# Performance work log

Measured on AMD Instinct MI355X. Metric: run time of the kernel, lower is better.

Reference implementation:

```python
import jax, jax.numpy as jnp
import numpy as np

SEQ, BS, H, I, E = 2048, 4, 2048, 4096, 8


def setup_inputs() -> dict:
    key = jax.random.key(0)
    ks = jax.random.split(key, 5)
    s = 0.02
    return {
        "hidden_states": jax.random.normal(ks[0], (SEQ, BS, H), dtype=jnp.float32),
        "router_w": jax.random.normal(ks[1], (H, E), dtype=jnp.float32) * s,
        "gate_w": jax.random.normal(ks[2], (E, H, I), dtype=jnp.float32) * s,
        "up_w": jax.random.normal(ks[3], (E, H, I), dtype=jnp.float32) * s,
        "down_w": jax.random.normal(ks[4], (E, I, H), dtype=jnp.float32) * s,
    }


def reference(hidden_states, router_w, gate_w, up_w, down_w):
    # Router: [S,B,H] @ [H,E] -> [S,B,E]; top-1 routing (num_experts_per_tok == 1)
    router_logits = jnp.einsum("sbh,he->sbe", hidden_states, router_w)
    routing_indices = jnp.argmax(router_logits, axis=-1)  # [S,B]
    # sigmoid routing weights are computed but NOT applied in the original combine
    routing_weights = jax.nn.sigmoid(jnp.max(router_logits, axis=-1))  # noqa: F841

    out = jnp.zeros_like(hidden_states)
    for e in range(E):  # small fixed expert count
        mask = (routing_indices == e)[..., None]  # [S,B,1]
        g = jnp.einsum("sbh,hi->sbi", hidden_states, gate_w[e])
        u = jnp.einsum("sbh,hi->sbi", hidden_states, up_w[e])
        y = jnp.einsum("sbi,ih->sbh", jax.nn.silu(g) * u, down_w[e])
        out = out + jnp.where(mask, y, jnp.zeros((), out.dtype))
    return out
```

## Files before the change

### kernel.cpp

```cpp
#include <hip/hip_runtime.h>
#include <hip/hip_bf16.h>

#define T_TOKENS 8192
#define H_DIM 2048
#define I_DIM 4096
#define E_EXP 8
#define PAD_ROWS 9216

typedef __bf16 bf16x8 __attribute__((ext_vector_type(8)));
typedef float floatx4 __attribute__((ext_vector_type(4)));
typedef unsigned short ushort8 __attribute__((ext_vector_type(8)));

__device__ __forceinline__ unsigned short f2bf(float f) {
  union { float f; unsigned int i; } c; c.f = f;
  unsigned int x = c.i;
  unsigned int r = x + 0x7fffu + ((x >> 16) & 1u);
  return (unsigned short)(r >> 16);
}

__device__ __forceinline__ float bf2float(unsigned short u) {
  union { unsigned int i; float f; } c; c.i = ((unsigned int)u) << 16;
  return c.f;
}

__device__ __forceinline__ void gload_lds16(const void* g, void* l) {
  __builtin_amdgcn_global_load_lds(
      (const __attribute__((address_space(1))) void*)g,
      (__attribute__((address_space(3))) void*)l, 16, 0, 0);
}

__global__ __launch_bounds__(256) void xcvt_kernel(const float* __restrict__ x,
                                                   unsigned short* __restrict__ xb,
                                                   int* __restrict__ hdr) {
  if (blockIdx.x == 0 && threadIdx.x < 32) hdr[threadIdx.x] = 0;
  int i = (blockIdx.x * 256 + threadIdx.x) * 4;
  floatx4 v = *(const floatx4*)(x + i);
  unsigned short o0 = f2bf(v[0]), o1 = f2bf(v[1]), o2 = f2bf(v[2]), o3 = f2bf(v[3]);
  ushort4 o; o.x = o0; o.y = o1; o.z = o2; o.w = o3;
  *(ushort4*)(xb + i) = o;
}

__global__ __launch_bounds__(256) void router_kernel(const float* __restrict__ x,
                                                     const float* __restrict__ rw,
                                                     int* __restrict__ idx,
                                                     int* __restrict__ hdr) {
  int lane = threadIdx.x & 63;
  int t = blockIdx.x * 4 + (threadIdx.x >> 6);
  const float* xr = x + (size_t)t * H_DIM;
  float acc[8];
#pragma unroll
  for (int e = 0; e < 8; ++e) acc[e] = 0.f;
  for (int i = lane; i < H_DIM; i += 64) {
    float h = xr[i];
    floatx4 r0 = *(const floatx4*)(rw + i * 8);
    floatx4 r1 = *(const floatx4*)(rw + i * 8 + 4);
#pragma unroll
    for (int e = 0; e < 4; ++e) { acc[e] += h * r0[e]; acc[e + 4] += h * r1[e]; }
  }
#pragma unroll
  for (int off = 32; off > 0; off >>= 1)
#pragma unroll
    for (int e = 0; e < 8; ++e) acc[e] += __shfl_xor(acc[e], off, 64);
  if (lane == 0) {
    int best = 0; float bv = acc[0];
#pragma unroll
    for (int e = 1; e < 8; ++e) if (acc[e] > bv) { bv = acc[e]; best = e; }
    idx[t] = best;
    atomicAdd(&hdr[best], 1);
  }
}

__global__ __launch_bounds__(256) void setup_kernel(int* __restrict__ hdr,
                                                    int* __restrict__ rows) {
  if (threadIdx.x == 0) {
    int b = 0;
    for (int e = 0; e < 8; ++e) {
      hdr[16 + e] = b;
      b += ((hdr[e] + 127) >> 7) << 7;
    }
  }
  for (int i = threadIdx.x; i < PAD_ROWS; i += 256) rows[i] = -1;
}

__global__ __launch_bounds__(256) void scatter_kernel(const int* __restrict__ idx,
                                                      int* __restrict__ hdr,
                                                      int* __restrict__ rows) {
  int t = blockIdx.x * 256 + threadIdx.x;
  int e = idx[t];
  int p = atomicAdd(&hdr[8 + e], 1);
  rows[hdr[16 + e] + p] = t;
}

template <int K, int N>
__global__ __launch_bounds__(256) void wtrans_kernel(const float* __restrict__ W,
                                                     unsigned short* __restrict__ Wt) {
  const int e = blockIdx.z;
  const int bn = blockIdx.x * 256;
  const int bk = blockIdx.y * 64;
  const float* Wp = W + (size_t)e * K * N;
  unsigned short* Wtp = Wt + (size_t)e * N * K;
  const int tid = threadIdx.x;
  const int n0 = (tid & 31) * 8;
  const int k0 = (tid >> 5) * 8;

  const float* src = Wp + (size_t)(bk + k0) * N + bn + n0;
  floatx4 a[8][2];
#pragma unroll
  for (int kk = 0; kk < 8; ++kk) {
    a[kk][0] = *(const floatx4*)(src + (size_t)kk * N);
    a[kk][1] = *(const floatx4*)(src + (size_t)kk * N + 4);
  }
  unsigned short* dst = Wtp + (size_t)(bn + n0) * K + bk + k0;
#pragma unroll
  for (int nn = 0; nn < 8; ++nn) {
    ushort8 o;
#pragma unroll
    for (int kk = 0; kk < 8; ++kk) o[kk] = f2bf(a[kk][nn >> 2][nn & 3]);
    *(ushort8*)(dst + (size_t)nn * K) = o;
  }
}

__global__ __launch_bounds__(256, 2) void moe_gemm_gu(
    const unsigned short* __restrict__ A,
    const unsigned short* __restrict__ Bg,
    const unsigned short* __restrict__ Bu,
    const int* __restrict__ hdr,
    const int* __restrict__ rows,
    unsigned short* __restrict__ inter) {
  const int e = blockIdx.z;
  const int cnt = hdr[e];
  if ((int)blockIdx.y * 128 >= cnt) return;
  const int seg = hdr[16 + e];

  const int tid = threadIdx.x;
  const int lane = tid & 63;
  const int wv = tid >> 6;
  const int wm = (wv & 1) * 64;
  const int wn = (wv >> 1) * 64;
  const int q = lane >> 4;
  const int l15 = lane & 15;

  __shared__ unsigned short sA[128 * 64];
  __shared__ unsigned short sBg[128 * 64];
  __shared__ unsigned short sBu[128 * 64];

  const int lr = lane >> 3;
  const int colsw = (lane & 7) ^ lr;
  const unsigned short* aptr[4];
  const unsigned short* bgptr[4];
  const unsigned short* buptr[4];
  const unsigned short* BgE = Bg + (size_t)e * I_DIM * H_DIM;
  const unsigned short* BuE = Bu + (size_t)e * I_DIM * H_DIM;
#pragma unroll
  for (int j = 0; j < 4; ++j) {
    const int R = j * 32 + wv * 8 + lr;
    int ar = rows[seg + blockIdx.y * 128 + R];
    if (ar < 0) ar = 0;
    aptr[j] = A + (size_t)ar * H_DIM + colsw * 8;
    bgptr[j] = BgE + (size_t)(blockIdx.x * 128 + R) * H_DIM + colsw * 8;
    buptr[j] = BuE + (size_t)(blockIdx.x * 128 + R) * H_DIM + colsw * 8;
  }

  floatx4 accg[4][4], accu[4][4];
#pragma unroll
  for (int a = 0; a < 4; ++a)
#pragma unroll
    for (int b = 0; b < 4; ++b) {
      accg[a][b] = (floatx4){0.f, 0.f, 0.f, 0.f};
      accu[a][b] = (floatx4){0.f, 0.f, 0.f, 0.f};
    }

  for (int kt = 0; kt < H_DIM; kt += 64) {
#pragma unroll
    for (int j = 0; j < 4; ++j) {
      gload_lds16(aptr[j] + kt, sA + (j * 32 + wv * 8) * 64);
      gload_lds16(bgptr[j] + kt, sBg + (j * 32 + wv * 8) * 64);
      gload_lds16(buptr[j] + kt, sBu + (j * 32 + wv * 8) * 64);
    }
    __syncthreads();
#pragma unroll
    for (int ks = 0; ks < 64; ks += 32) {
      const int sbase = ks >> 3;
      bf16x8 af[4], bfr[4];
#pragma unroll
      for (int fm = 0; fm < 4; ++fm) {
        const int ra = wm + fm * 16 + l15;
        af[fm] = __builtin_bit_cast(bf16x8,
            *(const ushort8*)(sA + ra * 64 + (((q + sbase) ^ (ra & 7)) << 3)));
      }
#pragma unroll
      for (int fn = 0; fn < 4; ++fn) {
        const int rb = wn + fn * 16 + l15;
        bfr[fn] = __builtin_bit_cast(bf16x8,
            *(const ushort8*)(sBg + rb * 64 + (((q + sbase) ^ (rb & 7)) << 3)));
      }
#pragma unroll
      for (int fm = 0; fm < 4; ++fm)
#pragma unroll
        for (int fn = 0; fn < 4; ++fn)
          accg[fm][fn] = __builtin_amdgcn_mfma_f32_16x16x32_bf16(af[fm], bfr[fn],
                                                                 accg[fm][fn], 0, 0, 0);
#pragma unroll
      for (int fn = 0; fn < 4; ++fn) {
        const int rb = wn + fn * 16 + l15;
        bfr[fn] = __builtin_bit_cast(bf16x8,
            *(const ushort8*)(sBu + rb * 64 + (((q + sbase) ^ (rb & 7)) << 3)));
      }
#pragma unroll
      for (int fm = 0; fm < 4; ++fm)
#pragma unroll
        for (int fn = 0; fn < 4; ++fn)
          accu[fm][fn] = __builtin_amdgcn_mfma_f32_16x16x32_bf16(af[fm], bfr[fn],
                                                                 accu[fm][fn], 0, 0, 0);
    }
    __syncthreads();
  }

#pragma unroll
  for (int fm = 0; fm < 4; ++fm)
#pragma unroll
    for (int fn = 0; fn < 4; ++fn)
#pragma unroll
      for (int rr = 0; rr < 4; ++rr) {
        const int row = wm + fm * 16 + q * 4 + rr;
        const int col = wn + fn * 16 + l15;
        const int gm = blockIdx.y * 128 + row;
        const int gn = blockIdx.x * 128 + col;
        const float g = accg[fm][fn][rr];
        const float u = accu[fm][fn][rr];
        const float s = g / (1.f + __expf(-g));
        inter[(size_t)(seg + gm) * I_DIM + gn] = f2bf(s * u);
      }
}

__global__ __launch_bounds__(256) void moe_gemm_down(
    const unsigned short* __restrict__ A,
    const unsigned short* __restrict__ Bt,
    const int* __restrict__ hdr,
    const int* __restrict__ rows,
    float* __restrict__ outp) {
  const int e = blockIdx.z;
  const int cnt = hdr[e];
  if ((int)blockIdx.y * 128 >= cnt) return;
  const int seg = hdr[16 + e];

  const int tid = threadIdx.x;
  const int lane = tid & 63;
  const int wv = tid >> 6;
  const int wm = (wv & 1) * 64;
  const int wn = (wv >> 1) * 64;
  const int q = lane >> 4;
  const int l15 = lane & 15;

  __shared__ unsigned short sA[128 * 64];
  __shared__ unsigned short sB[128 * 64];

  const int lr = lane >> 3;
  const int colsw = (lane & 7) ^ lr;
  const unsigned short* aptr[4];
  const unsigned short* bptr[4];
  const unsigned short* Be = Bt + (size_t)e * H_DIM * I_DIM;
#pragma unroll
  for (int j = 0; j < 4; ++j) {
    const int R = j * 32 + wv * 8 + lr;
    aptr[j] = A + (size_t)(seg + blockIdx.y * 128 + R) * I_DIM + colsw * 8;
    bptr[j] = Be + (size_t)(blockIdx.x * 128 + R) * I_DIM + colsw * 8;
  }

  floatx4 acc[4][4];
#pragma unroll
  for (int a = 0; a < 4; ++a)
#pragma unroll
    for (int b = 0; b < 4; ++b) acc[a][b] = (floatx4){0.f, 0.f, 0.f, 0.f};

  for (int kt = 0; kt < I_DIM; kt += 64) {
#pragma unroll
    for (int j = 0; j < 4; ++j) {
      gload_lds16(aptr[j] + kt, sA + (j * 32 + wv * 8) * 64);
      gload_lds16(bptr[j] + kt, sB + (j * 32 + wv * 8) * 64);
    }
    __syncthreads();
#pragma unroll
    for (int ks = 0; ks < 64; ks += 32) {
      const int sbase = ks >> 3;
      bf16x8 af[4], bfr[4];
#pragma unroll
      for (int fm = 0; fm < 4; ++fm) {
        const int ra = wm + fm * 16 + l15;
        af[fm] = __builtin_bit_cast(bf16x8,
            *(const ushort8*)(sA + ra * 64 + (((q + sbase) ^ (ra & 7)) << 3)));
      }
#pragma unroll
      for (int fn = 0; fn < 4; ++fn) {
        const int rb = wn + fn * 16 + l15;
        bfr[fn] = __builtin_bit_cast(bf16x8,
            *(const ushort8*)(sB + rb * 64 + (((q + sbase) ^ (rb & 7)) << 3)));
      }
#pragma unroll
      for (int fm = 0; fm < 4; ++fm)
#pragma unroll
        for (int fn = 0; fn < 4; ++fn)
          acc[fm][fn] = __builtin_amdgcn_mfma_f32_16x16x32_bf16(af[fm], bfr[fn],
                                                                acc[fm][fn], 0, 0, 0);
    }
    __syncthreads();
  }

#pragma unroll
  for (int fm = 0; fm < 4; ++fm)
#pragma unroll
    for (int fn = 0; fn < 4; ++fn)
#pragma unroll
      for (int rr = 0; rr < 4; ++rr) {
        const int row = wm + fm * 16 + q * 4 + rr;
        const int col = wn + fn * 16 + l15;
        const int gm = blockIdx.y * 128 + row;
        const int gn = blockIdx.x * 128 + col;
        const int tok = rows[seg + gm];
        if (tok >= 0) outp[(size_t)tok * H_DIM + gn] = acc[fm][fn][rr];
      }
}

extern "C" void kernel_launch(void* const* d_in, const int* in_sizes, int n_in,
                              void* d_out, int out_size, void* d_ws, size_t ws_size,
                              hipStream_t stream) {
  const float* hidden   = (const float*)d_in[0];
  const float* router_w = (const float*)d_in[1];
  const float* gate_w   = (const float*)d_in[2];
  const float* up_w     = (const float*)d_in[3];
  const float* down_w   = (const float*)d_in[4];
  float* out = (float*)d_out;

  char* ws = (char*)d_ws;
  int* hdr  = (int*)ws;
  int* idx  = (int*)(ws + 1024);
  int* rows = (int*)(ws + 33792);
  unsigned short* x_bf  = (unsigned short*)(ws + 70656);
  unsigned short* inter = (unsigned short*)(ws + 33625088);
  unsigned short* W1    = (unsigned short*)(ws + 109122560);
  unsigned short* W2    = (unsigned short*)(ws + 243340288);
  unsigned short* downt = W1;

  xcvt_kernel<<<T_TOKENS * H_DIM / 1024, 256, 0, stream>>>(hidden, x_bf, hdr);
  router_kernel<<<T_TOKENS / 4, 256, 0, stream>>>(hidden, router_w, idx, hdr);
  setup_kernel<<<1, 256, 0, stream>>>(hdr, rows);
  scatter_kernel<<<T_TOKENS / 256, 256, 0, stream>>>(idx, hdr, rows);

  wtrans_kernel<H_DIM, I_DIM><<<dim3(I_DIM / 256, H_DIM / 64, E_EXP), 256, 0, stream>>>(gate_w, W1);
  wtrans_kernel<H_DIM, I_DIM><<<dim3(I_DIM / 256, H_DIM / 64, E_EXP), 256, 0, stream>>>(up_w, W2);

  moe_gemm_gu<<<dim3(I_DIM / 128, 64, E_EXP), 256, 0, stream>>>(
      x_bf, W1, W2, hdr, rows, inter);

  wtrans_kernel<I_DIM, H_DIM><<<dim3(H_DIM / 256, I_DIM / 64, E_EXP), 256, 0, stream>>>(down_w, downt);
  moe_gemm_down<<<dim3(H_DIM / 128, 64, E_EXP), 256, 0, stream>>>(
      inter, downt, hdr, rows, out);
}
```

Before: 1.549 ms.

## Transpose weights via LDS tile and widen down-GEMM tile to 128x256

The weight transpose/convert kernel now stages a 64x64 tile in swizzled shared memory, so global reads are coalesced float4 rows and global writes are coalesced 16-byte rows. The old version wrote scattered 16-byte chunks with a large stride. The down-projection GEMM now computes two 128-column B tiles per block, reusing each A tile across twice the output width. This halves A reloads and block count. It raises register and LDS use (two accumulator sets, extra sB buffer) and sets launch bounds to 2 waves per EU, which may limit occupancy.

```diff
diff --git a/kernel.cpp b/kernel.cpp
--- a/kernel.cpp
+++ b/kernel.cpp
@@ -94,29 +94,42 @@
 template <int K, int N>
 __global__ __launch_bounds__(256) void wtrans_kernel(const float* __restrict__ W,
                                                      unsigned short* __restrict__ Wt) {
+  __shared__ unsigned short tile[64 * 64];
   const int e = blockIdx.z;
-  const int bn = blockIdx.x * 256;
+  const int bn = blockIdx.x * 64;
   const int bk = blockIdx.y * 64;
-  const float* Wp = W + (size_t)e * K * N;
-  unsigned short* Wtp = Wt + (size_t)e * N * K;
+  const float* Wp = W + (size_t)e * K * N + (size_t)bk * N + bn;
+  unsigned short* Wtp = Wt + (size_t)e * N * K + (size_t)bn * K + bk;
   const int tid = threadIdx.x;
-  const int n0 = (tid & 31) * 8;
-  const int k0 = (tid >> 5) * 8;
-
-  const float* src = Wp + (size_t)(bk + k0) * N + bn + n0;
-  floatx4 a[8][2];
-#pragma unroll
-  for (int kk = 0; kk < 8; ++kk) {
-    a[kk][0] = *(const floatx4*)(src + (size_t)kk * N);
-    a[kk][1] = *(const floatx4*)(src + (size_t)kk * N + 4);
-  }
-  unsigned short* dst = Wtp + (size_t)(bn + n0) * K + bk + k0;
-#pragma unroll
-  for (int nn = 0; nn < 8; ++nn) {
-    ushort8 o;
-#pragma unroll
-    for (int kk = 0; kk < 8; ++kk) o[kk] = f2bf(a[kk][nn >> 2][nn & 3]);
-    *(ushort8*)(dst + (size_t)nn * K) = o;
+
+  {
+    const int kq = tid >> 4;
+    const int nq = tid & 15;
+    floatx4 v[4];
+#pragma unroll
+    for (int i = 0; i < 4; ++i)
+      v[i] = *(const floatx4*)(Wp + (size_t)(kq * 4 + i) * N + nq * 4);
+    const int s16 = kq >> 1;
+    const int half = kq & 1;
+#pragma unroll
+    for (int j = 0; j < 4; ++j) {
+      const int n = nq * 4 + j;
+      ushort4 t;
+      t.x = f2bf(v[0][j]); t.y = f2bf(v[1][j]);
+      t.z = f2bf(v[2][j]); t.w = f2bf(v[3][j]);
+      *(ushort4*)(tile + n * 64 + ((s16 ^ (n & 7)) << 3) + half * 4) = t;
+    }
+  }
+  __syncthreads();
+  {
+    const int kc = tid & 7;
+    const int nr = tid >> 3;
+#pragma unroll
+    for (int it = 0; it < 2; ++it) {
+      const int n = it * 32 + nr;
+      ushort8 o = *(const ushort8*)(tile + n * 64 + ((kc ^ (n & 7)) << 3));
+      *(ushort8*)(Wtp + (size_t)n * K + kc * 8) = o;
+    }
   }
 }
 
@@ -233,7 +246,7 @@
       }
 }
 
-__global__ __launch_bounds__(256) void moe_gemm_down(
+__global__ __launch_bounds__(256, 2) void moe_gemm_down(
     const unsigned short* __restrict__ A,
     const unsigned short* __restrict__ Bt,
     const int* __restrict__ hdr,
@@ -253,31 +266,38 @@
   const int l15 = lane & 15;
 
   __shared__ unsigned short sA[128 * 64];
-  __shared__ unsigned short sB[128 * 64];
+  __shared__ unsigned short sB0[128 * 64];
+  __shared__ unsigned short sB1[128 * 64];
 
   const int lr = lane >> 3;
   const int colsw = (lane & 7) ^ lr;
   const unsigned short* aptr[4];
-  const unsigned short* bptr[4];
+  const unsigned short* b0ptr[4];
+  const unsigned short* b1ptr[4];
   const unsigned short* Be = Bt + (size_t)e * H_DIM * I_DIM;
 #pragma unroll
   for (int j = 0; j < 4; ++j) {
     const int R = j * 32 + wv * 8 + lr;
-    aptr[j] = A + (size_t)(seg + blockIdx.y * 128 + R) * I_DIM + colsw * 8;
-    bptr[j] = Be + (size_t)(blockIdx.x * 128 + R) * I_DIM + colsw * 8;
-  }
-
-  floatx4 acc[4][4];
+    aptr[j]  = A + (size_t)(seg + blockIdx.y * 128 + R) * I_DIM + colsw * 8;
+    b0ptr[j] = Be + (size_t)(blockIdx.x * 256 + R) * I_DIM + colsw * 8;
+    b1ptr[j] = Be + (size_t)(blockIdx.x * 256 + 128 + R) * I_DIM + colsw * 8;
+  }
+
+  floatx4 acc0[4][4], acc1[4][4];
 #pragma unroll
   for (int a = 0; a < 4; ++a)
 #pragma unroll
-    for (int b = 0; b < 4; ++b) acc[a][b] = (floatx4){0.f, 0.f, 0.f, 0.f};
+    for (int b = 0; b < 4; ++b) {
+      acc0[a][b] = (floatx4){0.f, 0.f, 0.f, 0.f};
+      acc1[a][b] = (floatx4){0.f, 0.f, 0.f, 0.f};
+    }
 
   for (int kt = 0; kt < I_DIM; kt += 64) {
 #pragma unroll
     for (int j = 0; j < 4; ++j) {
       gload_lds16(aptr[j] + kt, sA + (j * 32 + wv * 8) * 64);
-      gload_lds16(bptr[j] + kt, sB + (j * 32 + wv * 8) * 64);
+      gload_lds16(b0ptr[j] + kt, sB0 + (j * 32 + wv * 8) * 64);
+      gload_lds16(b1ptr[j] + kt, sB1 + (j * 32 + wv * 8) * 64);
     }
     __syncthreads();
 #pragma unroll
@@ -294,14 +314,26 @@
       for (int fn = 0; fn < 4; ++fn) {
         const int rb = wn + fn * 16 + l15;
         bfr[fn] = __builtin_bit_cast(bf16x8,
-            *(const ushort8*)(sB + rb * 64 + (((q + sbase) ^ (rb & 7)) << 3)));
+            *(const ushort8*)(sB0 + rb * 64 + (((q + sbase) ^ (rb & 7)) << 3)));
       }
 #pragma unroll
       for (int fm = 0; fm < 4; ++fm)
 #pragma unroll
         for (int fn = 0; fn < 4; ++fn)
-          acc[fm][fn] = __builtin_amdgcn_mfma_f32_16x16x32_bf16(af[fm], bfr[fn],
-                                                                acc[fm][fn], 0, 0, 0);
+          acc0[fm][fn] = __builtin_amdgcn_mfma_f32_16x16x32_bf16(af[fm], bfr[fn],
+                                                                 acc0[fm][fn], 0, 0, 0);
+#pragma unroll
+      for (int fn = 0; fn < 4; ++fn) {
+        const int rb = wn + fn * 16 + l15;
+        bfr[fn] = __builtin_bit_cast(bf16x8,
+            *(const ushort8*)(sB1 + rb * 64 + (((q + sbase) ^ (rb & 7)) << 3)));
+      }
+#pragma unroll
+      for (int fm = 0; fm < 4; ++fm)
+#pragma unroll
+        for (int fn = 0; fn < 4; ++fn)
+          acc1[fm][fn] = __builtin_amdgcn_mfma_f32_16x16x32_bf16(af[fm], bfr[fn],
+                                                                 acc1[fm][fn], 0, 0, 0);
     }
     __syncthreads();
   }
@@ -309,16 +341,18 @@
 #pragma unroll
   for (int fm = 0; fm < 4; ++fm)
 #pragma unroll
-    for (int fn = 0; fn < 4; ++fn)
-#pragma unroll
-      for (int rr = 0; rr < 4; ++rr) {
-        const int row = wm + fm * 16 + q * 4 + rr;
+    for (int rr = 0; rr < 4; ++rr) {
+      const int row = wm + fm * 16 + q * 4 + rr;
+      const int tok = rows[seg + blockIdx.y * 128 + row];
+      if (tok < 0) continue;
+      float* orow = outp + (size_t)tok * H_DIM + blockIdx.x * 256;
+#pragma unroll
+      for (int fn = 0; fn < 4; ++fn) {
         const int col = wn + fn * 16 + l15;
-        const int gm = blockIdx.y * 128 + row;
-        const int gn = blockIdx.x * 128 + col;
-        const int tok = rows[seg + gm];
-        if (tok >= 0) outp[(size_t)tok * H_DIM + gn] = acc[fm][fn][rr];
-      }
+        orow[col]       = acc0[fm][fn][rr];
+        orow[128 + col] = acc1[fm][fn][rr];
+      }
+    }
 }
 
 extern "C" void kernel_launch(void* const* d_in, const int* in_sizes, int n_in,
@@ -346,13 +380,13 @@
   setup_kernel<<<1, 256, 0, stream>>>(hdr, rows);
   scatter_kernel<<<T_TOKENS / 256, 256, 0, stream>>>(idx, hdr, rows);
 
-  wtrans_kernel<H_DIM, I_DIM><<<dim3(I_DIM / 256, H_DIM / 64, E_EXP), 256, 0, stream>>>(gate_w, W1);
-  wtrans_kernel<H_DIM, I_DIM><<<dim3(I_DIM / 256, H_DIM / 64, E_EXP), 256, 0, stream>>>(up_w, W2);
+  wtrans_kernel<H_DIM, I_DIM><<<dim3(I_DIM / 64, H_DIM / 64, E_EXP), 256, 0, stream>>>(gate_w, W1);
+  wtrans_kernel<H_DIM, I_DIM><<<dim3(I_DIM / 64, H_DIM / 64, E_EXP), 256, 0, stream>>>(up_w, W2);
 
   moe_gemm_gu<<<dim3(I_DIM / 128, 64, E_EXP), 256, 0, stream>>>(
       x_bf, W1, W2, hdr, rows, inter);
 
-  wtrans_kernel<I_DIM, H_DIM><<<dim3(H_DIM / 256, I_DIM / 64, E_EXP), 256, 0, stream>>>(down_w, downt);
-  moe_gemm_down<<<dim3(H_DIM / 128, 64, E_EXP), 256, 0, stream>>>(
+  wtrans_kernel<I_DIM, H_DIM><<<dim3(H_DIM / 64, I_DIM / 64, E_EXP), 256, 0, stream>>>(down_w, downt);
+  moe_gemm_down<<<dim3(H_DIM / 256, 64, E_EXP), 256, 0, stream>>>(
       inter, downt, hdr, rows, out);
 }
```

After: 1.504 ms. -2.9%, faster.
